# Kernel optimization log

Measured on AMD Instinct MI355X. Metric: run time of the kernel, lower is better.

Reference implementation:

```python
import jax, jax.numpy as jnp
import numpy as np

N = 100000   # num_entities
R = 8        # num_relations
B = 8        # num_bases = min(R, 30)
D = 128      # hidden_dim == embedding_dim
E = 800000   # num_edges


def rgcn_layer(x, edge_index, edge_type, basis, comp, root, bias):
    """PyG-style RGCNConv with basis decomposition and per-relation mean aggregation.

    Mean aggregation is linear, so we aggregate raw source features per
    (dst, relation) segment first, then apply the relation transform once
    per (node, relation) instead of per edge.
    """
    n, r = x.shape[0], comp.shape[0]
    W = jnp.einsum('rb,bio->rio', comp, basis)          # [R, D_in, D_out]
    src, dst = edge_index[0], edge_index[1]
    seg = dst * r + edge_type                            # segment key per edge
    agg = jax.ops.segment_sum(x[src], seg, num_segments=n * r)          # [N*R, D_in]
    cnt = jax.ops.segment_sum(jnp.ones((src.shape[0],), x.dtype), seg,
                              num_segments=n * r)                        # [N*R]
    agg = (agg / jnp.maximum(cnt, 1.0)[:, None]).reshape(n, r, -1)       # [N, R, D_in]
    return jnp.einsum('nri,rio->no', agg, W) + x @ root + bias


def setup_inputs() -> dict:
    key = jax.random.key(0)
    ks = jax.random.split(key, 12)
    s_in = 1.0 / np.sqrt(D)
    inp = {
        'edge_index': jax.random.randint(ks[0], (2, E), 0, N, dtype=jnp.int64 if jax.config.jax_enable_x64 else jnp.int32),
        'edge_type': jax.random.randint(ks[1], (E,), 0, R, dtype=jnp.int64 if jax.config.jax_enable_x64 else jnp.int32),
        'emb': jax.random.normal(ks[2], (N, D), jnp.float32) * s_in,
        'basis1': jax.random.normal(ks[3], (B, D, D), jnp.float32) * s_in,
        'comp1': jax.random.normal(ks[4], (R, B), jnp.float32) * (1.0 / np.sqrt(B)),
        'root1': jax.random.normal(ks[5], (D, D), jnp.float32) * s_in,
        'bias1': jnp.zeros((D,), jnp.float32),
        'basis2': jax.random.normal(ks[6], (B, D, D), jnp.float32) * s_in,
        'comp2': jax.random.normal(ks[7], (R, B), jnp.float32) * (1.0 / np.sqrt(B)),
        'root2': jax.random.normal(ks[8], (D, D), jnp.float32) * s_in,
        'bias2': jnp.zeros((D,), jnp.float32),
    }
    return inp


def reference(edge_index, edge_type, emb, basis1, comp1, root1, bias1,
              basis2, comp2, root2, bias2):
    # layer 1 + ReLU (dropout is identity at eval time)
    x = rgcn_layer(emb, edge_index, edge_type, basis1, comp1, root1, bias1)
    x = jax.nn.relu(x)
    # layer 2 (output layer, no activation)
    x = rgcn_layer(x, edge_index, edge_type, basis2, comp2, root2, bias2)
    return x
```

## Files before the change

### kernel.cpp

```cpp
#include <hip/hip_runtime.h>

#define NN 100000
#define RR 8
#define BB 8
#define DD 128
#define EE 800000
#define KT 1152
#define NBLK 782
#define NSEG2 (NBLK * 1024)
#define ASTR 40
#define AGSTR 132

typedef __attribute__((ext_vector_type(8))) __bf16 bf16x8;
typedef __attribute__((ext_vector_type(4))) float f32x4;
typedef __attribute__((ext_vector_type(4))) unsigned int u32x4;

__device__ __forceinline__ unsigned short f2bf(float f) {
    unsigned u = __float_as_uint(f);
    u += 0x7fffu + ((u >> 16) & 1u);
    return (unsigned short)(u >> 16);
}
__device__ __forceinline__ float bf2f(unsigned short h) {
    return __uint_as_float(((unsigned)h) << 16);
}

__global__ __launch_bounds__(256) void k_cvt(const float* __restrict__ x,
                                             unsigned short* __restrict__ xh) {
    int i = blockIdx.x * 256 + threadIdx.x;
    f32x4 a = ((const f32x4*)x)[2 * i];
    f32x4 b = ((const f32x4*)x)[2 * i + 1];
    u32x4 o;
    o[0] = (unsigned)f2bf(a[0]) | ((unsigned)f2bf(a[1]) << 16);
    o[1] = (unsigned)f2bf(a[2]) | ((unsigned)f2bf(a[3]) << 16);
    o[2] = (unsigned)f2bf(b[0]) | ((unsigned)f2bf(b[1]) << 16);
    o[3] = (unsigned)f2bf(b[2]) | ((unsigned)f2bf(b[3]) << 16);
    ((u32x4*)xh)[i] = o;
}

__global__ __launch_bounds__(256) void k_cnt(const int* __restrict__ ei,
                                             const int* __restrict__ et,
                                             int* __restrict__ cnt) {
    int e = blockIdx.x * 256 + threadIdx.x;
    if (e < EE) {
        int d = ei[EE + e];
        atomicAdd(&cnt[(d >> 7) * 1024 + et[e] * 128 + (d & 127)], 1);
    }
}

__global__ __launch_bounds__(256) void k_scan_local(const int* __restrict__ cnt,
                                                    int* __restrict__ loc,
                                                    int* __restrict__ bsum) {
    __shared__ int tmp[256];
    int t = threadIdx.x, i = blockIdx.x * 256 + t;
    int v = cnt[i];
    tmp[t] = v; __syncthreads();
    int val = v;
#pragma unroll
    for (int d = 1; d < 256; d <<= 1) {
        int a = (t >= d) ? tmp[t - d] : 0;
        __syncthreads();
        val += a; tmp[t] = val;
        __syncthreads();
    }
    loc[i] = val - v;
    if (t == 255) bsum[blockIdx.x] = val;
}

__global__ void k_scan_bsum(const int* __restrict__ bsum, int* __restrict__ boff) {
    __shared__ int tmp[256];
    const int NB = NSEG2 / 256;
    const int CH = 13;
    int t = threadIdx.x;
    int base = t * CH, s = 0;
    for (int j = 0; j < CH; ++j) { int idx = base + j; if (idx < NB) s += bsum[idx]; }
    tmp[t] = s; __syncthreads();
    int val = s;
#pragma unroll
    for (int d = 1; d < 256; d <<= 1) {
        int a = (t >= d) ? tmp[t - d] : 0;
        __syncthreads();
        val += a; tmp[t] = val;
        __syncthreads();
    }
    int run = val - s;
    for (int j = 0; j < CH; ++j) { int idx = base + j; if (idx < NB) { boff[idx] = run; run += bsum[idx]; } }
}

__global__ __launch_bounds__(256) void k_scan_add(int* __restrict__ loc,
                                                  const int* __restrict__ boff) {
    int i = blockIdx.x * 256 + threadIdx.x;
    loc[i] += boff[i >> 8];
}

__global__ __launch_bounds__(256) void k_scatter(const int* __restrict__ ei,
                                                 const int* __restrict__ et,
                                                 int* __restrict__ segoff,
                                                 int* __restrict__ spk) {
    int e = blockIdx.x * 256 + threadIdx.x;
    if (e < EE) {
        int d = ei[EE + e];
        int key = (d >> 7) * 1024 + et[e] * 128 + (d & 127);
        int pos = atomicAdd(&segoff[key], 1);
        spk[pos] = ei[e];
    }
}

__global__ __launch_bounds__(256) void k_prepB(const float* __restrict__ root,
                                               const float* __restrict__ comp,
                                               const float* __restrict__ basis,
                                               unsigned short* __restrict__ Bhi,
                                               unsigned short* __restrict__ Blo) {
    int idx = blockIdx.x * 256 + threadIdx.x;
    if (idx >= DD * KT) return;
    int o = idx / KT, k = idx - o * KT;
    float v;
    if (k < DD) {
        v = root[k * DD + o];
    } else {
        int r = (k - DD) >> 7, i = (k - DD) & 127;
        float s = 0.f;
#pragma unroll
        for (int b = 0; b < BB; ++b)
            s += comp[r * BB + b] * basis[((size_t)b * DD + i) * DD + o];
        v = s;
    }
    unsigned short hi = f2bf(v);
    Bhi[idx] = hi;
    Blo[idx] = f2bf(v - bf2f(hi));
}

template <bool WRITE_H1>
__global__ __launch_bounds__(256, 3) void k_gemm(
    const unsigned short* __restrict__ xh,
    const unsigned short* __restrict__ Bhi,
    const unsigned short* __restrict__ Blo,
    const float* __restrict__ bias,
    const int* __restrict__ spk,
    const int* __restrict__ segend,
    const int* __restrict__ cnt,
    unsigned short* __restrict__ h1h,
    float* __restrict__ outf)
{
    __shared__ unsigned short Aagg[128 * AGSTR];
    __shared__ unsigned short Bhs[128 * ASTR];
    __shared__ unsigned short Bls[128 * ASTR];

    const int tid = threadIdx.x;
    const int b = blockIdx.x;
    const int M0 = b * 128;

    const int wave = tid >> 6, lane = tid & 63;
    const int quad = lane >> 4, lm = lane & 15;
    const int node = tid >> 1, half = tid & 1;

    f32x4 acc[2][8];
#pragma unroll
    for (int a = 0; a < 2; ++a)
#pragma unroll
        for (int n = 0; n < 8; ++n) acc[a][n] = (f32x4){0.f, 0.f, 0.f, 0.f};

    const int bro0 = tid >> 2;
    const int bro1 = 64 + (tid >> 2);
    const int bq8 = (tid & 3) * 8;
    u32x4 bh0, bh1, bl0, bl1;

    auto bload = [&](int k0) {
        bh0 = *(const u32x4*)(Bhi + (size_t)bro0 * KT + k0 + bq8);
        bl0 = *(const u32x4*)(Blo + (size_t)bro0 * KT + k0 + bq8);
        bh1 = *(const u32x4*)(Bhi + (size_t)bro1 * KT + k0 + bq8);
        bl1 = *(const u32x4*)(Blo + (size_t)bro1 * KT + k0 + bq8);
    };
    auto bwrite = [&]() {
        *(u32x4*)&Bhs[bro0 * ASTR + bq8] = bh0;
        *(u32x4*)&Bls[bro0 * ASTR + bq8] = bl0;
        *(u32x4*)&Bhs[bro1 * ASTR + bq8] = bh1;
        *(u32x4*)&Bls[bro1 * ASTR + bq8] = bl1;
    };

    auto kstep = [&](bf16x8 af0, bf16x8 af1, int k0next, bool tail) {
#pragma unroll
        for (int nt = 0; nt < 8; ++nt) {
            bf16x8 bh = __builtin_bit_cast(bf16x8, *(const u32x4*)&Bhs[(nt * 16 + lm) * ASTR + quad * 8]);
            bf16x8 bl = __builtin_bit_cast(bf16x8, *(const u32x4*)&Bls[(nt * 16 + lm) * ASTR + quad * 8]);
            acc[0][nt] = __builtin_amdgcn_mfma_f32_16x16x32_bf16(af0, bh, acc[0][nt], 0, 0, 0);
            acc[0][nt] = __builtin_amdgcn_mfma_f32_16x16x32_bf16(af0, bl, acc[0][nt], 0, 0, 0);
            acc[1][nt] = __builtin_amdgcn_mfma_f32_16x16x32_bf16(af1, bh, acc[1][nt], 0, 0, 0);
            acc[1][nt] = __builtin_amdgcn_mfma_f32_16x16x32_bf16(af1, bl, acc[1][nt], 0, 0, 0);
        }
        if (tail) return;
        __syncthreads();
        bwrite();
        if (k0next >= 0) bload(k0next);
        __syncthreads();
    };

    bload(0);
    bwrite();
    bload(32);

    int r0 = M0 + wave * 32 + lm;      if (r0 > NN - 1) r0 = NN - 1;
    int r1 = M0 + wave * 32 + 16 + lm; if (r1 > NN - 1) r1 = NN - 1;
    const unsigned short* pa0 = xh + (size_t)r0 * DD + quad * 8;
    const unsigned short* pa1 = xh + (size_t)r1 * DD + quad * 8;

    __syncthreads();

#pragma unroll
    for (int ks = 0; ks < 4; ++ks) {
        bf16x8 af0 = __builtin_bit_cast(bf16x8, *(const u32x4*)(pa0 + ks * 32));
        bf16x8 af1 = __builtin_bit_cast(bf16x8, *(const u32x4*)(pa1 + ks * 32));
        const int k0n = (ks < 2) ? (ks + 2) * 32 : DD + (ks - 2) * 32;
        kstep(af0, af1, k0n, false);
    }

    for (int r = 0; r < RR; ++r) {
        const int gix = b * 1024 + r * 128 + node;
        const int send_ = segend[gix];
        const int cs = cnt[gix];
        const int beg = send_ - cs;

#pragma unroll
        for (int p = 0; p < 2; ++p) {
            const int coff = half * 64 + p * 32;
            float vlo[16], vhi[16];
#pragma unroll
            for (int j = 0; j < 16; ++j) { vlo[j] = 0.f; vhi[j] = 0.f; }
            for (int t = 0; t < cs; ++t) {
                const int sp = spk[beg + t];
                const u32x4* ps = (const u32x4*)(xh + (size_t)sp * DD + coff);
                u32x4 c0 = ps[0], c1 = ps[1], c2 = ps[2], c3 = ps[3];
#pragma unroll
                for (int w = 0; w < 4; ++w) {
                    vlo[w]      += __uint_as_float(c0[w] << 16);
                    vhi[w]      += __uint_as_float(c0[w] & 0xFFFF0000u);
                    vlo[4 + w]  += __uint_as_float(c1[w] << 16);
                    vhi[4 + w]  += __uint_as_float(c1[w] & 0xFFFF0000u);
                    vlo[8 + w]  += __uint_as_float(c2[w] << 16);
                    vhi[8 + w]  += __uint_as_float(c2[w] & 0xFFFF0000u);
                    vlo[12 + w] += __uint_as_float(c3[w] << 16);
                    vhi[12 + w] += __uint_as_float(c3[w] & 0xFFFF0000u);
                }
            }
            const float inv = 1.0f / (float)(cs > 1 ? cs : 1);
            unsigned pk[16];
#pragma unroll
            for (int j = 0; j < 16; ++j)
                pk[j] = (unsigned)f2bf(vlo[j] * inv) | ((unsigned)f2bf(vhi[j] * inv) << 16);
            unsigned short* pw = &Aagg[node * AGSTR + coff];
            *(u32x4*)(pw + 0)  = (u32x4){pk[0],  pk[1],  pk[2],  pk[3]};
            *(u32x4*)(pw + 8)  = (u32x4){pk[4],  pk[5],  pk[6],  pk[7]};
            *(u32x4*)(pw + 16) = (u32x4){pk[8],  pk[9],  pk[10], pk[11]};
            *(u32x4*)(pw + 24) = (u32x4){pk[12], pk[13], pk[14], pk[15]};
        }

        __syncthreads();

#pragma unroll
        for (int s = 0; s < 4; ++s) {
            bf16x8 af0 = __builtin_bit_cast(bf16x8,
                *(const u32x4*)&Aagg[(wave * 32 + lm) * AGSTR + s * 32 + quad * 8]);
            bf16x8 af1 = __builtin_bit_cast(bf16x8,
                *(const u32x4*)&Aagg[(wave * 32 + 16 + lm) * AGSTR + s * 32 + quad * 8]);
            const bool tail = (r == RR - 1) && (s == 3);
            const int k0n = (s < 2) ? DD + r * 128 + (s + 2) * 32
                          : ((r < RR - 1) ? DD + (r + 1) * 128 + (s - 2) * 32 : -1);
            kstep(af0, af1, k0n, tail);
        }
    }

#pragma unroll
    for (int mt = 0; mt < 2; ++mt) {
#pragma unroll
        for (int nt = 0; nt < 8; ++nt) {
            const float bvn = bias[nt * 16 + lm];
#pragma unroll
            for (int rg = 0; rg < 4; ++rg) {
                int row = M0 + wave * 32 + mt * 16 + quad * 4 + rg;
                if (row < NN) {
                    int col = nt * 16 + lm;
                    float v = acc[mt][nt][rg] + bvn;
                    if (WRITE_H1) h1h[(size_t)row * DD + col] = f2bf(fmaxf(v, 0.f));
                    else          outf[(size_t)row * DD + col] = v;
                }
            }
        }
    }
}


extern "C" void kernel_launch(void* const* d_in, const int* in_sizes, int n_in,
                              void* d_out, int out_size, void* d_ws, size_t ws_size,
                              hipStream_t stream) {
    const int*   ei     = (const int*)d_in[0];
    const int*   et     = (const int*)d_in[1];
    const float* emb    = (const float*)d_in[2];
    const float* basis1 = (const float*)d_in[3];
    const float* comp1  = (const float*)d_in[4];
    const float* root1  = (const float*)d_in[5];
    const float* bias1  = (const float*)d_in[6];
    const float* basis2 = (const float*)d_in[7];
    const float* comp2  = (const float*)d_in[8];
    const float* root2  = (const float*)d_in[9];
    const float* bias2  = (const float*)d_in[10];
    float* out = (float*)d_out;
    (void)in_sizes; (void)n_in; (void)out_size; (void)ws_size;

    char* ws = (char*)d_ws;
    int*            cnt    = (int*)(ws + 0);
    int*            segoff = (int*)(ws + 3203072);
    int*            spk    = (int*)(ws + 6406144);
    int*            bsum   = (int*)(ws + 9606144);
    int*            boff   = (int*)(ws + 9618656);
    unsigned short* Bhi1   = (unsigned short*)(ws + 9656320);
    unsigned short* Blo1   = (unsigned short*)(ws + 9951232);
    unsigned short* Bhi2   = (unsigned short*)(ws + 10246144);
    unsigned short* Blo2   = (unsigned short*)(ws + 10541056);
    unsigned short* embh   = (unsigned short*)(ws + 10835968);
    unsigned short* h1h    = (unsigned short*)(ws + 36435968);

    hipMemsetAsync(cnt, 0, (size_t)NSEG2 * 4, stream);

    k_cvt       <<<NN * DD / (256 * 8), 256, 0, stream>>>(emb, embh);
    k_cnt       <<<(EE + 255) / 256, 256, 0, stream>>>(ei, et, cnt);
    k_scan_local<<<NSEG2 / 256, 256, 0, stream>>>(cnt, segoff, bsum);
    k_scan_bsum <<<1, 256, 0, stream>>>(bsum, boff);
    k_scan_add  <<<NSEG2 / 256, 256, 0, stream>>>(segoff, boff);
    k_scatter   <<<(EE + 255) / 256, 256, 0, stream>>>(ei, et, segoff, spk);

    k_prepB<<<(DD * KT + 255) / 256, 256, 0, stream>>>(root1, comp1, basis1, Bhi1, Blo1);
    k_prepB<<<(DD * KT + 255) / 256, 256, 0, stream>>>(root2, comp2, basis2, Bhi2, Blo2);

    k_gemm<true> <<<NBLK, 256, 0, stream>>>(embh, Bhi1, Blo1, bias1, spk, segoff, cnt, h1h, nullptr);
    k_gemm<false><<<NBLK, 256, 0, stream>>>(h1h,  Bhi2, Blo2, bias2, spk, segoff, cnt, nullptr, out);
}
```

Measured before the change: 575.8 us.

## Fuse prep kernels, stage segment metadata in LDS, swizzle B tiles, halve aggregation buffer

Merges the bf16 conversion, edge counting and both weight-prep kernels into one launch to cut launch overhead. In the GEMM kernel, per-block segment offsets, counts and source indices are staged in LDS, and the B tiles use an XOR swizzle instead of padding to avoid bank conflicts. The aggregation buffer is halved so each 64-column half is aggregated and consumed in turn, and the gather loop is unrolled by two edges to raise memory-level parallelism. The extra LDS for the index arrays may lower occupancy, and the split adds more barriers per relation.

```diff
diff --git a/kernel.cpp b/kernel.cpp
--- a/kernel.cpp
+++ b/kernel.cpp
@@ -8,8 +8,11 @@
 #define KT 1152
 #define NBLK 782
 #define NSEG2 (NBLK * 1024)
-#define ASTR 40
-#define AGSTR 132
+#define AGSTR 68
+#define SPKCAP 1664
+#define NCVT 6250
+#define NCNT 3125
+#define NPB  576
 
 typedef __attribute__((ext_vector_type(8))) __bf16 bf16x8;
 typedef __attribute__((ext_vector_type(4))) float f32x4;
@@ -24,26 +27,61 @@
     return __uint_as_float(((unsigned)h) << 16);
 }
 
-__global__ __launch_bounds__(256) void k_cvt(const float* __restrict__ x,
-                                             unsigned short* __restrict__ xh) {
-    int i = blockIdx.x * 256 + threadIdx.x;
-    f32x4 a = ((const f32x4*)x)[2 * i];
-    f32x4 b = ((const f32x4*)x)[2 * i + 1];
-    u32x4 o;
-    o[0] = (unsigned)f2bf(a[0]) | ((unsigned)f2bf(a[1]) << 16);
-    o[1] = (unsigned)f2bf(a[2]) | ((unsigned)f2bf(a[3]) << 16);
-    o[2] = (unsigned)f2bf(b[0]) | ((unsigned)f2bf(b[1]) << 16);
-    o[3] = (unsigned)f2bf(b[2]) | ((unsigned)f2bf(b[3]) << 16);
-    ((u32x4*)xh)[i] = o;
-}
-
-__global__ __launch_bounds__(256) void k_cnt(const int* __restrict__ ei,
-                                             const int* __restrict__ et,
-                                             int* __restrict__ cnt) {
-    int e = blockIdx.x * 256 + threadIdx.x;
-    if (e < EE) {
-        int d = ei[EE + e];
-        atomicAdd(&cnt[(d >> 7) * 1024 + et[e] * 128 + (d & 127)], 1);
+__device__ __forceinline__ void prepB_body(int idx,
+                                           const float* __restrict__ root,
+                                           const float* __restrict__ comp,
+                                           const float* __restrict__ basis,
+                                           unsigned short* __restrict__ Bhi,
+                                           unsigned short* __restrict__ Blo) {
+    if (idx >= DD * KT) return;
+    int o = idx / KT, k = idx - o * KT;
+    float v;
+    if (k < DD) {
+        v = root[k * DD + o];
+    } else {
+        int r = (k - DD) >> 7, i = (k - DD) & 127;
+        float s = 0.f;
+#pragma unroll
+        for (int b = 0; b < BB; ++b)
+            s += comp[r * BB + b] * basis[((size_t)b * DD + i) * DD + o];
+        v = s;
+    }
+    unsigned short hi = f2bf(v);
+    Bhi[idx] = hi;
+    Blo[idx] = f2bf(v - bf2f(hi));
+}
+
+__global__ __launch_bounds__(256) void k_pre(
+    const float* __restrict__ x, unsigned short* __restrict__ xh,
+    const int* __restrict__ ei, const int* __restrict__ et, int* __restrict__ cnt,
+    const float* __restrict__ root1, const float* __restrict__ comp1,
+    const float* __restrict__ basis1,
+    unsigned short* __restrict__ Bhi1, unsigned short* __restrict__ Blo1,
+    const float* __restrict__ root2, const float* __restrict__ comp2,
+    const float* __restrict__ basis2,
+    unsigned short* __restrict__ Bhi2, unsigned short* __restrict__ Blo2)
+{
+    const int blk = blockIdx.x, tid = threadIdx.x;
+    if (blk < NCVT) {
+        int i = blk * 256 + tid;
+        f32x4 a = ((const f32x4*)x)[2 * i];
+        f32x4 b = ((const f32x4*)x)[2 * i + 1];
+        u32x4 o;
+        o[0] = (unsigned)f2bf(a[0]) | ((unsigned)f2bf(a[1]) << 16);
+        o[1] = (unsigned)f2bf(a[2]) | ((unsigned)f2bf(a[3]) << 16);
+        o[2] = (unsigned)f2bf(b[0]) | ((unsigned)f2bf(b[1]) << 16);
+        o[3] = (unsigned)f2bf(b[2]) | ((unsigned)f2bf(b[3]) << 16);
+        ((u32x4*)xh)[i] = o;
+    } else if (blk < NCVT + NCNT) {
+        int e = (blk - NCVT) * 256 + tid;
+        if (e < EE) {
+            int d = ei[EE + e];
+            atomicAdd(&cnt[(d >> 7) * 1024 + et[e] * 128 + (d & 127)], 1);
+        }
+    } else if (blk < NCVT + NCNT + NPB) {
+        prepB_body((blk - NCVT - NCNT) * 256 + tid, root1, comp1, basis1, Bhi1, Blo1);
+    } else {
+        prepB_body((blk - NCVT - NCNT - NPB) * 256 + tid, root2, comp2, basis2, Bhi2, Blo2);
     }
 }
 
@@ -103,30 +141,6 @@
         int pos = atomicAdd(&segoff[key], 1);
         spk[pos] = ei[e];
     }
-}
-
-__global__ __launch_bounds__(256) void k_prepB(const float* __restrict__ root,
-                                               const float* __restrict__ comp,
-                                               const float* __restrict__ basis,
-                                               unsigned short* __restrict__ Bhi,
-                                               unsigned short* __restrict__ Blo) {
-    int idx = blockIdx.x * 256 + threadIdx.x;
-    if (idx >= DD * KT) return;
-    int o = idx / KT, k = idx - o * KT;
-    float v;
-    if (k < DD) {
-        v = root[k * DD + o];
-    } else {
-        int r = (k - DD) >> 7, i = (k - DD) & 127;
-        float s = 0.f;
-#pragma unroll
-        for (int b = 0; b < BB; ++b)
-            s += comp[r * BB + b] * basis[((size_t)b * DD + i) * DD + o];
-        v = s;
-    }
-    unsigned short hi = f2bf(v);
-    Bhi[idx] = hi;
-    Blo[idx] = f2bf(v - bf2f(hi));
 }
 
 template <bool WRITE_H1>
@@ -142,12 +156,30 @@
     float* __restrict__ outf)
 {
     __shared__ unsigned short Aagg[128 * AGSTR];
-    __shared__ unsigned short Bhs[128 * ASTR];
-    __shared__ unsigned short Bls[128 * ASTR];
+    __shared__ unsigned short Bhs[128 * 32];
+    __shared__ unsigned short Bls[128 * 32];
+    __shared__ int sbeg[1024];
+    __shared__ unsigned short scnt[1024];
+    __shared__ int spkl[SPKCAP];
 
     const int tid = threadIdx.x;
     const int b = blockIdx.x;
     const int M0 = b * 128;
+    const int gbase = b * 1024;
+
+#pragma unroll
+    for (int p = 0; p < 4; ++p) {
+        int i = p * 256 + tid;
+        int end = segend[gbase + i];
+        int c = cnt[gbase + i];
+        sbeg[i] = end - c;
+        scnt[i] = (unsigned short)c;
+    }
+    const int beg0 = segend[gbase] - cnt[gbase];
+    const int bend = segend[gbase + 1023];
+    const int ecount = bend - beg0;
+    const bool useLds = (ecount <= SPKCAP);
+    if (useLds) for (int i = tid; i < ecount; i += 256) spkl[i] = spk[beg0 + i];
 
     const int wave = tid >> 6, lane = tid & 63;
     const int quad = lane >> 4, lm = lane & 15;
@@ -159,29 +191,30 @@
 #pragma unroll
         for (int n = 0; n < 8; ++n) acc[a][n] = (f32x4){0.f, 0.f, 0.f, 0.f};
 
-    const int bro0 = tid >> 2;
-    const int bro1 = 64 + (tid >> 2);
-    const int bq8 = (tid & 3) * 8;
+    const int bro = tid >> 2;
+    const int bq = tid & 3;
+    const int bsw = bq ^ ((bro >> 1) & 3);
+    const int brd = lm * 32 + (quad ^ ((lm >> 1) & 3)) * 8;
     u32x4 bh0, bh1, bl0, bl1;
 
     auto bload = [&](int k0) {
-        bh0 = *(const u32x4*)(Bhi + (size_t)bro0 * KT + k0 + bq8);
-        bl0 = *(const u32x4*)(Blo + (size_t)bro0 * KT + k0 + bq8);
-        bh1 = *(const u32x4*)(Bhi + (size_t)bro1 * KT + k0 + bq8);
-        bl1 = *(const u32x4*)(Blo + (size_t)bro1 * KT + k0 + bq8);
+        bh0 = *(const u32x4*)(Bhi + (size_t)bro * KT + k0 + bq * 8);
+        bl0 = *(const u32x4*)(Blo + (size_t)bro * KT + k0 + bq * 8);
+        bh1 = *(const u32x4*)(Bhi + (size_t)(64 + bro) * KT + k0 + bq * 8);
+        bl1 = *(const u32x4*)(Blo + (size_t)(64 + bro) * KT + k0 + bq * 8);
     };
     auto bwrite = [&]() {
-        *(u32x4*)&Bhs[bro0 * ASTR + bq8] = bh0;
-        *(u32x4*)&Bls[bro0 * ASTR + bq8] = bl0;
-        *(u32x4*)&Bhs[bro1 * ASTR + bq8] = bh1;
-        *(u32x4*)&Bls[bro1 * ASTR + bq8] = bl1;
+        *(u32x4*)&Bhs[bro * 32 + bsw * 8] = bh0;
+        *(u32x4*)&Bls[bro * 32 + bsw * 8] = bl0;
+        *(u32x4*)&Bhs[(64 + bro) * 32 + bsw * 8] = bh1;
+        *(u32x4*)&Bls[(64 + bro) * 32 + bsw * 8] = bl1;
     };
 
     auto kstep = [&](bf16x8 af0, bf16x8 af1, int k0next, bool tail) {
 #pragma unroll
         for (int nt = 0; nt < 8; ++nt) {
-            bf16x8 bh = __builtin_bit_cast(bf16x8, *(const u32x4*)&Bhs[(nt * 16 + lm) * ASTR + quad * 8]);
-            bf16x8 bl = __builtin_bit_cast(bf16x8, *(const u32x4*)&Bls[(nt * 16 + lm) * ASTR + quad * 8]);
+            bf16x8 bh = __builtin_bit_cast(bf16x8, *(const u32x4*)&Bhs[nt * 512 + brd]);
+            bf16x8 bl = __builtin_bit_cast(bf16x8, *(const u32x4*)&Bls[nt * 512 + brd]);
             acc[0][nt] = __builtin_amdgcn_mfma_f32_16x16x32_bf16(af0, bh, acc[0][nt], 0, 0, 0);
             acc[0][nt] = __builtin_amdgcn_mfma_f32_16x16x32_bf16(af0, bl, acc[0][nt], 0, 0, 0);
             acc[1][nt] = __builtin_amdgcn_mfma_f32_16x16x32_bf16(af1, bh, acc[1][nt], 0, 0, 0);
@@ -214,57 +247,81 @@
     }
 
     for (int r = 0; r < RR; ++r) {
-        const int gix = b * 1024 + r * 128 + node;
-        const int send_ = segend[gix];
-        const int cs = cnt[gix];
-        const int beg = send_ - cs;
-
-#pragma unroll
-        for (int p = 0; p < 2; ++p) {
-            const int coff = half * 64 + p * 32;
+        const int si = r * 128 + node;
+        const int beg = sbeg[si];
+        const int cs = (int)scnt[si];
+        const int lb = beg - beg0;
+
+#pragma unroll
+        for (int h = 0; h < 2; ++h) {
+            const int coff = h * 64 + half * 32;
+
             float vlo[16], vhi[16];
 #pragma unroll
             for (int j = 0; j < 16; ++j) { vlo[j] = 0.f; vhi[j] = 0.f; }
-            for (int t = 0; t < cs; ++t) {
-                const int sp = spk[beg + t];
-                const u32x4* ps = (const u32x4*)(xh + (size_t)sp * DD + coff);
-                u32x4 c0 = ps[0], c1 = ps[1], c2 = ps[2], c3 = ps[3];
+
+            int t = 0;
+            for (; t + 1 < cs; t += 2) {
+                const int sp0 = useLds ? spkl[lb + t]     : spk[beg + t];
+                const int sp1 = useLds ? spkl[lb + t + 1] : spk[beg + t + 1];
+                const u32x4* p0 = (const u32x4*)(xh + (size_t)sp0 * DD + coff);
+                const u32x4* p1 = (const u32x4*)(xh + (size_t)sp1 * DD + coff);
+                u32x4 a0 = p0[0], a1 = p0[1], a2 = p0[2], a3 = p0[3];
+                u32x4 b0 = p1[0], b1 = p1[1], b2 = p1[2], b3 = p1[3];
 #pragma unroll
                 for (int w = 0; w < 4; ++w) {
-                    vlo[w]      += __uint_as_float(c0[w] << 16);
-                    vhi[w]      += __uint_as_float(c0[w] & 0xFFFF0000u);
-                    vlo[4 + w]  += __uint_as_float(c1[w] << 16);
-                    vhi[4 + w]  += __uint_as_float(c1[w] & 0xFFFF0000u);
-                    vlo[8 + w]  += __uint_as_float(c2[w] << 16);
-                    vhi[8 + w]  += __uint_as_float(c2[w] & 0xFFFF0000u);
-                    vlo[12 + w] += __uint_as_float(c3[w] << 16);
-                    vhi[12 + w] += __uint_as_float(c3[w] & 0xFFFF0000u);
+                    vlo[w]      += __uint_as_float(a0[w] << 16) + __uint_as_float(b0[w] << 16);
+                    vhi[w]      += __uint_as_float(a0[w] & 0xFFFF0000u) + __uint_as_float(b0[w] & 0xFFFF0000u);
+                    vlo[4 + w]  += __uint_as_float(a1[w] << 16) + __uint_as_float(b1[w] << 16);
+                    vhi[4 + w]  += __uint_as_float(a1[w] & 0xFFFF0000u) + __uint_as_float(b1[w] & 0xFFFF0000u);
+                    vlo[8 + w]  += __uint_as_float(a2[w] << 16) + __uint_as_float(b2[w] << 16);
+                    vhi[8 + w]  += __uint_as_float(a2[w] & 0xFFFF0000u) + __uint_as_float(b2[w] & 0xFFFF0000u);
+                    vlo[12 + w] += __uint_as_float(a3[w] << 16) + __uint_as_float(b3[w] << 16);
+                    vhi[12 + w] += __uint_as_float(a3[w] & 0xFFFF0000u) + __uint_as_float(b3[w] & 0xFFFF0000u);
                 }
             }
+            if (t < cs) {
+                const int sp0 = useLds ? spkl[lb + t] : spk[beg + t];
+                const u32x4* p0 = (const u32x4*)(xh + (size_t)sp0 * DD + coff);
+                u32x4 a0 = p0[0], a1 = p0[1], a2 = p0[2], a3 = p0[3];
+#pragma unroll
+                for (int w = 0; w < 4; ++w) {
+                    vlo[w]      += __uint_as_float(a0[w] << 16);
+                    vhi[w]      += __uint_as_float(a0[w] & 0xFFFF0000u);
+                    vlo[4 + w]  += __uint_as_float(a1[w] << 16);
+                    vhi[4 + w]  += __uint_as_float(a1[w] & 0xFFFF0000u);
+                    vlo[8 + w]  += __uint_as_float(a2[w] << 16);
+                    vhi[8 + w]  += __uint_as_float(a2[w] & 0xFFFF0000u);
+                    vlo[12 + w] += __uint_as_float(a3[w] << 16);
+                    vhi[12 + w] += __uint_as_float(a3[w] & 0xFFFF0000u);
+                }
+            }
+
             const float inv = 1.0f / (float)(cs > 1 ? cs : 1);
             unsigned pk[16];
 #pragma unroll
             for (int j = 0; j < 16; ++j)
                 pk[j] = (unsigned)f2bf(vlo[j] * inv) | ((unsigned)f2bf(vhi[j] * inv) << 16);
-            unsigned short* pw = &Aagg[node * AGSTR + coff];
+            unsigned short* pw = &Aagg[node * AGSTR + half * 32];
             *(u32x4*)(pw + 0)  = (u32x4){pk[0],  pk[1],  pk[2],  pk[3]};
             *(u32x4*)(pw + 8)  = (u32x4){pk[4],  pk[5],  pk[6],  pk[7]};
             *(u32x4*)(pw + 16) = (u32x4){pk[8],  pk[9],  pk[10], pk[11]};
             *(u32x4*)(pw + 24) = (u32x4){pk[12], pk[13], pk[14], pk[15]};
-        }
-
-        __syncthreads();
-
-#pragma unroll
-        for (int s = 0; s < 4; ++s) {
-            bf16x8 af0 = __builtin_bit_cast(bf16x8,
-                *(const u32x4*)&Aagg[(wave * 32 + lm) * AGSTR + s * 32 + quad * 8]);
-            bf16x8 af1 = __builtin_bit_cast(bf16x8,
-                *(const u32x4*)&Aagg[(wave * 32 + 16 + lm) * AGSTR + s * 32 + quad * 8]);
-            const bool tail = (r == RR - 1) && (s == 3);
-            const int k0n = (s < 2) ? DD + r * 128 + (s + 2) * 32
-                          : ((r < RR - 1) ? DD + (r + 1) * 128 + (s - 2) * 32 : -1);
-            kstep(af0, af1, k0n, tail);
+
+            __syncthreads();
+
+#pragma unroll
+            for (int s2 = 0; s2 < 2; ++s2) {
+                const int s = 2 * h + s2;
+                bf16x8 af0 = __builtin_bit_cast(bf16x8,
+                    *(const u32x4*)&Aagg[(wave * 32 + lm) * AGSTR + s2 * 32 + quad * 8]);
+                bf16x8 af1 = __builtin_bit_cast(bf16x8,
+                    *(const u32x4*)&Aagg[(wave * 32 + 16 + lm) * AGSTR + s2 * 32 + quad * 8]);
+                const bool tail = (r == RR - 1) && (s == 3);
+                const int k0n = (s < 2) ? DD + r * 128 + (s + 2) * 32
+                              : ((r < RR - 1) ? DD + (r + 1) * 128 + (s - 2) * 32 : -1);
+                kstep(af0, af1, k0n, tail);
+            }
         }
     }
 
@@ -320,16 +377,16 @@
 
     hipMemsetAsync(cnt, 0, (size_t)NSEG2 * 4, stream);
 
-    k_cvt       <<<NN * DD / (256 * 8), 256, 0, stream>>>(emb, embh);
-    k_cnt       <<<(EE + 255) / 256, 256, 0, stream>>>(ei, et, cnt);
+    k_pre<<<NCVT + NCNT + 2 * NPB, 256, 0, stream>>>(
+        emb, embh, ei, et, cnt,
+        root1, comp1, basis1, Bhi1, Blo1,
+        root2, comp2, basis2, Bhi2, Blo2);
+
     k_scan_local<<<NSEG2 / 256, 256, 0, stream>>>(cnt, segoff, bsum);
     k_scan_bsum <<<1, 256, 0, stream>>>(bsum, boff);
     k_scan_add  <<<NSEG2 / 256, 256, 0, stream>>>(segoff, boff);
     k_scatter   <<<(EE + 255) / 256, 256, 0, stream>>>(ei, et, segoff, spk);
 
-    k_prepB<<<(DD * KT + 255) / 256, 256, 0, stream>>>(root1, comp1, basis1, Bhi1, Blo1);
-    k_prepB<<<(DD * KT + 255) / 256, 256, 0, stream>>>(root2, comp2, basis2, Bhi2, Blo2);
-
     k_gemm<true> <<<NBLK, 256, 0, stream>>>(embh, Bhi1, Blo1, bias1, spk, segoff, cnt, h1h, nullptr);
     k_gemm<false><<<NBLK, 256, 0, stream>>>(h1h,  Bhi2, Blo2, bias2, spk, segoff, cnt, nullptr, out);
 }
```

Result: slower. 648.9 us (+12.7%).
